# Optimization experiments

Hardware: AMD Instinct MI355X
Metric: run time of the kernel (lower is better)

## Reference

```python
import jax, jax.numpy as jnp
import numpy as np

D_MODEL = 4096
N_HEADS = 32
N_KV_HEADS = 32
D_HEAD = 128
D_LATENT = 512
N_CKV = 4            # n_compressed_kv_heads = d_latent // d_head
T = 2048             # num_tokens (single-sequence prefill)
ROPE_BASE = 10000.0
NEG = -1e30


def _rope(x, positions):
    """Neox-style rotary embedding. x: (T, H, D)."""
    d = x.shape[-1]
    inv_freq = 1.0 / (ROPE_BASE ** (jnp.arange(0, d // 2, dtype=jnp.float32) * (2.0 / d)))
    freqs = positions.astype(jnp.float32)[:, None] * inv_freq[None, :]  # (T, D/2)
    cos = jnp.cos(freqs)[:, None, :]
    sin = jnp.sin(freqs)[:, None, :]
    x1, x2 = jnp.split(x, 2, axis=-1)
    return jnp.concatenate([x1 * cos - x2 * sin, x2 * cos + x1 * sin], axis=-1)


def setup_inputs() -> dict:
    key = jax.random.key(0)
    ks = jax.random.split(key, 6)
    s = jnp.float32(0.02)
    return {
        "positions": jnp.arange(T, dtype=jnp.int32),
        "hidden_states": jax.random.normal(ks[0], (T, D_MODEL), jnp.float32),
        "Wq": jax.random.normal(ks[1], (D_MODEL, N_HEADS * D_HEAD), jnp.float32) * s,
        "Wc": jax.random.normal(ks[2], (D_MODEL, 2 * D_LATENT), jnp.float32) * s,
        "Wuk": jax.random.normal(ks[3], (2 * D_LATENT, N_KV_HEADS * D_HEAD), jnp.float32) * s,
        "Wuv": jax.random.normal(ks[4], (2 * D_LATENT, N_KV_HEADS * D_HEAD), jnp.float32) * s,
        "Wo": jax.random.normal(ks[5], (N_HEADS * D_HEAD, D_MODEL), jnp.float32) * s,
    }


def reference(positions, hidden_states, Wq, Wc, Wuk, Wuv, Wo):
    # Q projection
    q = (hidden_states @ Wq).reshape(T, N_HEADS, D_HEAD)
    # MLA compression: hidden -> c_kv (2*d_latent), split into c_k / c_v
    c_kv = hidden_states @ Wc                                   # (T, 2*D_LATENT)
    c_k = c_kv[:, :D_LATENT].reshape(T, N_CKV, D_HEAD)          # compressed K cache
    c_v = c_kv[:, D_LATENT:].reshape(T, N_CKV, D_HEAD)          # compressed V cache
    # Decompression (computed by the source module; K is RoPE'd then discarded,
    # V is unused -- the v1 attention path runs over the compressed cache).
    K = (c_kv @ Wuk).reshape(T, N_KV_HEADS, D_HEAD)
    V = (c_kv @ Wuv).reshape(T, N_KV_HEADS, D_HEAD)             # noqa: unused, matches source
    # RoPE on q (and K, whose rotated value is dead in the source)
    q = _rope(q, positions)
    K = _rope(K, positions)  # dead, kept for FLOP parity with the source
    # GQA attention: n_heads=32 query heads over n_compressed_kv_heads=4 kv heads
    g = N_HEADS // N_CKV
    qg = q.reshape(T, N_CKV, g, D_HEAD)
    scale = jnp.float32(1.0 / np.sqrt(D_HEAD))
    scores = jnp.einsum('tkgd,skd->kgts', qg, c_k) * scale      # (N_CKV, g, T, T)
    causal = positions[:, None] >= positions[None, :]           # (T, T)
    scores = jnp.where(causal[None, None], scores, NEG)
    probs = jax.nn.softmax(scores, axis=-1)
    ctx = jnp.einsum('kgts,skd->tkgd', probs, c_v).reshape(T, N_HEADS * D_HEAD)
    return ctx @ Wo
```

## Files before the change

### kernel.cpp

```cpp
#include <hip/hip_runtime.h>
#include <hip/hip_bf16.h>
#include <cstdint>
#include <cstddef>


typedef unsigned short u16;
typedef short s16x8 __attribute__((ext_vector_type(8)));
typedef short s16x4 __attribute__((ext_vector_type(4)));
typedef float f32x4 __attribute__((ext_vector_type(4)));

#define MFMA16(a, b, c) __builtin_amdgcn_mfma_f32_16x16x32_bf16((a), (b), (c), 0, 0, 0)

#define QSCALE 0.12751899f
#define LOG2_ROPE_BASE 13.287712379549449f
#define FIXMAX 24.0f

__device__ __forceinline__ u16 f2b(float f) {
  return __builtin_bit_cast(u16, __float2bfloat16(f));
}
__device__ __forceinline__ void async_copy16(u16* lds, const u16* g) {
  __builtin_amdgcn_global_load_lds(
      (const __attribute__((address_space(1))) unsigned int*)g,
      (__attribute__((address_space(3))) unsigned int*)lds, 16, 0, 0);
}

__global__ __launch_bounds__(256)
void prep_kernel(const float* __restrict__ hidden, const float* __restrict__ Wq,
                 const float* __restrict__ Wc, const float* __restrict__ Wo,
                 u16* __restrict__ hb, u16* __restrict__ WqT,
                 u16* __restrict__ WcT, u16* __restrict__ WoT) {
  __shared__ alignas(16) u16 tile[64 * 72];
  const int b = blockIdx.x;
  const int t = threadIdx.x;

  if (b >= 9216) {
    int i = (b - 9216) * 256 + t;
    const float4* p = (const float4*)hidden + (size_t)i * 2;
    float4 a = p[0], c = p[1];
    s16x8 v;
    v[0] = (short)f2b(a.x); v[1] = (short)f2b(a.y);
    v[2] = (short)f2b(a.z); v[3] = (short)f2b(a.w);
    v[4] = (short)f2b(c.x); v[5] = (short)f2b(c.y);
    v[6] = (short)f2b(c.z); v[7] = (short)f2b(c.w);
    *(s16x8*)&hb[(size_t)i * 8] = v;
    return;
  }

  const float* in;
  u16* out;
  int gx, in_ld, out_ld;
  if (b < 4096)      { in = Wq; out = WqT; gx = b;        in_ld = 4096; out_ld = 4096; }
  else if (b < 5120) { in = Wc; out = WcT; gx = b - 4096; in_ld = 1024; out_ld = 4096; }
  else               { in = Wo; out = WoT; gx = b - 5120; in_ld = 4096; out_ld = 4096; }
  const int nbx = in_ld / 64;
  const int c0 = (gx % nbx) * 64, r0 = (gx / nbx) * 64;
  const int rr = t >> 3, cc = (t & 7) * 8;
#pragma unroll
  for (int p = 0; p < 2; p++) {
    int row = p * 32 + rr;
    const float4* src = (const float4*)&in[(size_t)(r0 + row) * in_ld + c0 + cc];
    float4 a = src[0], c = src[1];
    s16x8 v;
    v[0] = (short)f2b(a.x); v[1] = (short)f2b(a.y);
    v[2] = (short)f2b(a.z); v[3] = (short)f2b(a.w);
    v[4] = (short)f2b(c.x); v[5] = (short)f2b(c.y);
    v[6] = (short)f2b(c.z); v[7] = (short)f2b(c.w);
    *(s16x8*)&tile[row * 72 + cc] = v;
  }
  __syncthreads();
#pragma unroll
  for (int p = 0; p < 2; p++) {
    int orow = p * 32 + rr;
    s16x8 v;
#pragma unroll
    for (int j = 0; j < 8; j++) v[j] = (short)tile[(cc + j) * 72 + orow];
    *(s16x8*)&out[(size_t)(c0 + orow) * out_ld + r0 + cc] = v;
  }
}

__global__ __launch_bounds__(256)
void transpose_ckv(const u16* __restrict__ in, u16* __restrict__ out) {
  __shared__ alignas(16) u16 tile[64 * 72];
  const int kh = blockIdx.z;
  const int c0 = blockIdx.x * 64, r0 = blockIdx.y * 64;
  const int in_off = 512 + kh * 128;
  u16* outk = out + (size_t)kh * 128 * 2048;
  const int t = threadIdx.x;
  const int rr = t >> 3, cc = (t & 7) * 8;
#pragma unroll
  for (int p = 0; p < 2; p++) {
    int row = p * 32 + rr;
    s16x8 v = *(const s16x8*)&in[(size_t)(r0 + row) * 1024 + in_off + c0 + cc];
    *(s16x8*)&tile[row * 72 + cc] = v;
  }
  __syncthreads();
#pragma unroll
  for (int p = 0; p < 2; p++) {
    int orow = p * 32 + rr;
    s16x8 v;
#pragma unroll
    for (int j = 0; j < 8; j++) v[j] = (short)tile[(cc + j) * 72 + orow];
    *(s16x8*)&outk[(size_t)(c0 + orow) * 2048 + r0 + cc] = v;
  }
}

template <int EPI>
__global__ __launch_bounds__(256, 3)
void gemm_bt(const u16* __restrict__ A, const u16* __restrict__ Bt,
             void* __restrict__ Cv, void* __restrict__ Cv2,
             const int* __restrict__ positions) {
  __shared__ alignas(16) u16 As[2][128 * 32];
  __shared__ alignas(16) u16 Bs[2][128 * 32];

  const int tid = threadIdx.x;
  const int w = tid >> 6, l = tid & 63;
  const int wm = w >> 1, wn = w & 1;
  const int lrow = l >> 4, lcol = l & 15;

  const int wgid = (int)blockIdx.y * (int)gridDim.x + (int)blockIdx.x;
  const int cpx = (int)gridDim.x >> 3;
  const int xk = wgid & 7, xr = wgid >> 3;
  const int bx = cpx * xk + xr % cpx, by = xr / cpx;
  const int m0 = by * 128, n0 = bx * 128;

  f32x4 acc[4][4] = {};

  const int srow = l >> 2;
  const int scol = ((l & 3) ^ ((l >> 3) & 3)) * 8;
  const int rxor = (lcol >> 1) & 3;
  const u16* Ag = A + (size_t)(m0 + w * 32 + srow) * 4096 + scol;
  const u16* Bg = Bt + (size_t)(n0 + w * 32 + srow) * 4096 + scol;

  for (int kt = 0; kt < 4096; kt += 64) {
    __syncthreads();
#pragma unroll
    for (int hf = 0; hf < 2; hf++) {
      async_copy16(&As[hf][(w * 32) * 32], Ag + kt + hf * 32);
      async_copy16(&As[hf][(w * 32 + 16) * 32],
                   Ag + (size_t)16 * 4096 + kt + hf * 32);
      async_copy16(&Bs[hf][(w * 32) * 32], Bg + kt + hf * 32);
      async_copy16(&Bs[hf][(w * 32 + 16) * 32],
                   Bg + (size_t)16 * 4096 + kt + hf * 32);
    }
    __syncthreads();

#pragma unroll
    for (int hf = 0; hf < 2; hf++) {
      s16x8 a[4], b[4];
#pragma unroll
      for (int i = 0; i < 4; i++)
        a[i] = *(const s16x8*)&As[hf][(wm * 64 + i * 16 + lcol) * 32 +
                                      (lrow ^ rxor) * 8];
#pragma unroll
      for (int j = 0; j < 4; j++)
        b[j] = *(const s16x8*)&Bs[hf][(wn * 32 + (j & 1) * 16 + (j >> 1) * 64 +
                                       lcol) * 32 + (lrow ^ rxor) * 8];
#pragma unroll
      for (int i = 0; i < 4; i++)
#pragma unroll
        for (int j = 0; j < 4; j++)
          acc[i][j] = MFMA16(a[i], b[j], acc[i][j]);
    }
  }

  if constexpr (EPI == 3) {
    float* C = (float*)Cv;
#pragma unroll
    for (int i = 0; i < 4; i++) {
      int row = m0 + wm * 64 + i * 16 + lrow * 4;
#pragma unroll
      for (int j = 0; j < 4; j++) {
        int col = n0 + wn * 32 + (j & 1) * 16 + (j >> 1) * 64 + lcol;
#pragma unroll
        for (int r = 0; r < 4; r++)
          C[(size_t)(row + r) * 4096 + col] = acc[i][j][r];
      }
    }
  } else {
    if (n0 >= 4096) {
      u16* C = (u16*)Cv2;
      int cb = n0 - 4096;
#pragma unroll
      for (int i = 0; i < 4; i++) {
        int row = m0 + wm * 64 + i * 16 + lrow * 4;
#pragma unroll
        for (int j = 0; j < 4; j++) {
          int col = cb + wn * 32 + (j & 1) * 16 + (j >> 1) * 64 + lcol;
#pragma unroll
          for (int r = 0; r < 4; r++)
            C[(size_t)(row + r) * 1024 + col] = f2b(acc[i][j][r]);
        }
      }
    } else {
      u16* C = (u16*)Cv;
      float inv[2];
#pragma unroll
      for (int j = 0; j < 2; j++) {
        int d = wn * 32 + j * 16 + lcol;
        inv[j] = exp2f((float)d * (-LOG2_ROPE_BASE / 64.f));
      }
#pragma unroll
      for (int i = 0; i < 4; i++) {
        int row = m0 + wm * 64 + i * 16 + lrow * 4;
#pragma unroll
        for (int r = 0; r < 4; r++) {
          float pos = (float)positions[row + r];
#pragma unroll
          for (int j = 0; j < 2; j++) {
            int d = wn * 32 + j * 16 + lcol;
            float ang = pos * inv[j];
            float sv, cv;
            sincosf(ang, &sv, &cv);
            float x1 = acc[i][j][r];
            float x2 = acc[i][j + 2][r];
            C[(size_t)(row + r) * 4096 + n0 + d] = f2b((x1 * cv - x2 * sv) * QSCALE);
            C[(size_t)(row + r) * 4096 + n0 + d + 64] =
                f2b((x2 * cv + x1 * sv) * QSCALE);
          }
        }
      }
    }
  }
}

__global__ __launch_bounds__(256, 4)
void attn_kernel(const u16* __restrict__ Q, const u16* __restrict__ ckv,
                 const u16* __restrict__ vT, u16* __restrict__ ctx) {
  __shared__ alignas(16) u16 Kt[2][4096];
  __shared__ alignas(16) u16 Vt[2][4096];
  __shared__ alignas(16) u16 Ps[4][512];

  const int tid = threadIdx.x, w = tid >> 6, l = tid & 63;
  const int lrow = l >> 4, lcol = l & 15;
  const int b = blockIdx.x;
  const int hg = b & 7;
  const int qi = b >> 3;
  const int ji = qi >> 5, ii = qi & 31;
  const int qt = (ji == 0) ? ii : (ji == 1) ? 63 - ii
               : (ji == 2) ? 64 + ii : 127 - ii;
  const int kh = hg >> 1;
  const int h = hg * 4 + w;
  const int nkt = (qt >> 1) + 1;
  const int sxor = (l >> 3) & 3;
  const int kxor = (lcol >> 1) & 3;

  const u16* kg0 = ckv + (size_t)(l >> 2) * 1024 + kh * 128 + w * 32 +
                   ((l & 3) ^ sxor) * 8;
  const u16* vg0 = vT + (size_t)(kh * 128 + w * 32 + (l >> 2)) * 2048 +
                   ((l & 3) ^ sxor) * 8;

  s16x8 qf[4];
  {
    const u16* qg = Q + (size_t)(qt * 16 + lcol) * 4096 + h * 128 + lrow * 8;
#pragma unroll
    for (int kc = 0; kc < 4; kc++)
      qf[kc] = *(const s16x8*)&qg[kc * 32];
  }

  f32x4 o[8] = {};
  float lsum = 0.f;

  {
    async_copy16(&Kt[0][w * 1024], kg0);
    async_copy16(&Kt[0][w * 1024 + 512], kg0 + (size_t)16 * 1024);
    async_copy16(&Vt[0][w * 1024], vg0);
    async_copy16(&Vt[0][w * 1024 + 512], vg0 + (size_t)16 * 2048);
  }
  asm volatile("s_waitcnt vmcnt(0)" ::: "memory");
  __syncthreads();

#pragma unroll 1
  for (int kt = 0; kt < nkt; kt++) {
    const int cur = kt & 1;
    if (kt + 1 < nkt) {
      const u16* kg = kg0 + (size_t)(kt + 1) * 32 * 1024;
      const u16* vg = vg0 + (size_t)(kt + 1) * 32;
      async_copy16(&Kt[cur ^ 1][w * 1024], kg);
      async_copy16(&Kt[cur ^ 1][w * 1024 + 512], kg + (size_t)16 * 1024);
      async_copy16(&Vt[cur ^ 1][w * 1024], vg);
      async_copy16(&Vt[cur ^ 1][w * 1024 + 512], vg + (size_t)16 * 2048);
    }

    f32x4 s[2] = {};
    __builtin_amdgcn_s_setprio(1);
#pragma unroll
    for (int kc = 0; kc < 4; kc++) {
#pragma unroll
      for (int mt = 0; mt < 2; mt++) {
        s16x8 ka = *(const s16x8*)&Kt[cur][kc * 1024 + (mt * 16 + lcol) * 32 +
                                          (lrow ^ kxor) * 8];
        s[mt] = MFMA16(ka, qf[kc], s[mt]);
      }
    }
    __builtin_amdgcn_s_setprio(0);

    if (kt == nkt - 1) {
      const int qloc = (qt & 1) * 16 + lcol;
#pragma unroll
      for (int mt = 0; mt < 2; mt++)
#pragma unroll
        for (int r = 0; r < 4; r++) {
          int key = mt * 16 + lrow * 4 + r;
          if (key > qloc) s[mt][r] = -1e30f;
        }
    }

#pragma unroll
    for (int mt = 0; mt < 2; mt++) {
      s16x4 pk;
#pragma unroll
      for (int r = 0; r < 4; r++) {
        float p = exp2f(s[mt][r] - FIXMAX);
        lsum += p;
        pk[r] = (short)f2b(p);
      }
      const int key32 = mt * 16 + lrow * 4;
      *(s16x4*)&Ps[w][lcol * 32 + (key32 ^ (kxor << 3))] = pk;
    }

    s16x8 pa = *(const s16x8*)&Ps[w][lcol * 32 + (lrow ^ kxor) * 8];
    __builtin_amdgcn_s_setprio(1);
#pragma unroll
    for (int ntO = 0; ntO < 8; ntO++) {
      s16x8 vb = *(const s16x8*)&Vt[cur][(ntO * 16 + lcol) * 32 +
                                         (lrow ^ kxor) * 8];
      o[ntO] = MFMA16(pa, vb, o[ntO]);
    }
    __builtin_amdgcn_s_setprio(0);

    asm volatile("s_waitcnt vmcnt(0)" ::: "memory");
    __syncthreads();
  }

  lsum += __shfl_xor(lsum, 16);
  lsum += __shfl_xor(lsum, 32);
  float* fl = (float*)&Ps[w][0];
  if (l < 16) fl[l] = 1.f / lsum;
  f32x4 lf = *(const f32x4*)&fl[lrow * 4];
#pragma unroll
  for (int ntO = 0; ntO < 8; ntO++)
#pragma unroll
    for (int r = 0; r < 4; r++) {
      int q = qt * 16 + lrow * 4 + r;
      int d = h * 128 + ntO * 16 + lcol;
      ctx[(size_t)q * 4096 + d] = f2b(o[ntO][r] * lf[r]);
    }
}

extern "C" void kernel_launch(void* const* d_in, const int* in_sizes, int n_in,
                              void* d_out, int out_size, void* d_ws, size_t ws_size,
                              hipStream_t stream) {
  const int* positions = (const int*)d_in[0];
  const float* hidden = (const float*)d_in[1];
  const float* Wq = (const float*)d_in[2];
  const float* Wc = (const float*)d_in[3];
  const float* Wo = (const float*)d_in[6];

  char* ws = (char*)d_ws;
  u16* hb  = (u16*)(ws);
  u16* WT  = (u16*)(ws + 16777216);
  u16* qbf = (u16*)(ws + 58720256);
  u16* ckv = (u16*)(ws + 75497472);
  u16* cvT = (u16*)(ws + 79691776);
  u16* WoT = (u16*)(ws + 81788928);
  u16* ctx = hb;

  dim3 blk(256);

  prep_kernel<<<dim3(13312), blk, 0, stream>>>(hidden, Wq, Wc, Wo, hb, WT,
                                               WT + (size_t)4096 * 4096, WoT);

  gemm_bt<1><<<dim3(40, 16), blk, 0, stream>>>(hb, WT, qbf, ckv, positions);

  transpose_ckv<<<dim3(2, 32, 4), blk, 0, stream>>>(ckv, cvT);

  attn_kernel<<<dim3(1024), blk, 0, stream>>>(qbf, ckv, cvT, ctx);

  gemm_bt<3><<<dim3(32, 16), blk, 0, stream>>>(ctx, WoT, d_out, nullptr,
                                               positions);
}
```

Baseline: 458.3 us.

## Replace GEMM with 256x256 8-wave pipelined kernel and fuse cV transpose

Rewrites the projection GEMMs as a 512-thread kernel with 256x256 tiles, double-buffered async LDS staging in four k/m sub-phases with explicit vmcnt waits, and MFMA priority raising. The first GEMM's epilogue now writes the V half of c_kv transposed straight into cvT, so the separate transpose kernel launch goes away. The aim is more data reuse per tile and overlap of loads with MFMA work. In exchange, grids become small (160 and 128 blocks) against the device's compute-unit count, which may leave units idle and cause tail effects.

After: 518.8 us. 1.13x slower.

```diff
diff --git a/kernel.cpp b/kernel.cpp
--- a/kernel.cpp
+++ b/kernel.cpp
@@ -78,114 +78,159 @@
   }
 }
 
-__global__ __launch_bounds__(256)
-void transpose_ckv(const u16* __restrict__ in, u16* __restrict__ out) {
-  __shared__ alignas(16) u16 tile[64 * 72];
-  const int kh = blockIdx.z;
-  const int c0 = blockIdx.x * 64, r0 = blockIdx.y * 64;
-  const int in_off = 512 + kh * 128;
-  u16* outk = out + (size_t)kh * 128 * 2048;
-  const int t = threadIdx.x;
-  const int rr = t >> 3, cc = (t & 7) * 8;
-#pragma unroll
-  for (int p = 0; p < 2; p++) {
-    int row = p * 32 + rr;
-    s16x8 v = *(const s16x8*)&in[(size_t)(r0 + row) * 1024 + in_off + c0 + cc];
-    *(s16x8*)&tile[row * 72 + cc] = v;
-  }
-  __syncthreads();
-#pragma unroll
-  for (int p = 0; p < 2; p++) {
-    int orow = p * 32 + rr;
-    s16x8 v;
-#pragma unroll
-    for (int j = 0; j < 8; j++) v[j] = (short)tile[(cc + j) * 72 + orow];
-    *(s16x8*)&outk[(size_t)(c0 + orow) * 2048 + r0 + cc] = v;
-  }
-}
-
 template <int EPI>
-__global__ __launch_bounds__(256, 3)
-void gemm_bt(const u16* __restrict__ A, const u16* __restrict__ Bt,
-             void* __restrict__ Cv, void* __restrict__ Cv2,
-             const int* __restrict__ positions) {
-  __shared__ alignas(16) u16 As[2][128 * 32];
-  __shared__ alignas(16) u16 Bs[2][128 * 32];
+__global__ __launch_bounds__(512, 2)
+void gemm8(const u16* __restrict__ A, const u16* __restrict__ Bt,
+           void* __restrict__ Cv, void* __restrict__ Cv2,
+           u16* __restrict__ CvT, const int* __restrict__ positions) {
+  __shared__ alignas(16) u16 As[2][2][256 * 32];
+  __shared__ alignas(16) u16 Bs[2][2][256 * 32];
 
   const int tid = threadIdx.x;
   const int w = tid >> 6, l = tid & 63;
-  const int wm = w >> 1, wn = w & 1;
+  const int wm = w >> 2, wn = w & 3;
   const int lrow = l >> 4, lcol = l & 15;
-
-  const int wgid = (int)blockIdx.y * (int)gridDim.x + (int)blockIdx.x;
-  const int cpx = (int)gridDim.x >> 3;
-  const int xk = wgid & 7, xr = wgid >> 3;
-  const int bx = cpx * xk + xr % cpx, by = xr / cpx;
-  const int m0 = by * 128, n0 = bx * 128;
-
-  f32x4 acc[4][4] = {};
-
-  const int srow = l >> 2;
-  const int scol = ((l & 3) ^ ((l >> 3) & 3)) * 8;
+  const int wgid = (int)blockIdx.x;
+  const int by = wgid & 7, bx = wgid >> 3;
+  const int m0 = by * 256, n0 = bx * 256;
   const int rxor = (lcol >> 1) & 3;
-  const u16* Ag = A + (size_t)(m0 + w * 32 + srow) * 4096 + scol;
-  const u16* Bg = Bt + (size_t)(n0 + w * 32 + srow) * 4096 + scol;
-
-  for (int kt = 0; kt < 4096; kt += 64) {
-    __syncthreads();
-#pragma unroll
-    for (int hf = 0; hf < 2; hf++) {
-      async_copy16(&As[hf][(w * 32) * 32], Ag + kt + hf * 32);
-      async_copy16(&As[hf][(w * 32 + 16) * 32],
-                   Ag + (size_t)16 * 4096 + kt + hf * 32);
-      async_copy16(&Bs[hf][(w * 32) * 32], Bg + kt + hf * 32);
-      async_copy16(&Bs[hf][(w * 32 + 16) * 32],
-                   Bg + (size_t)16 * 4096 + kt + hf * 32);
-    }
-    __syncthreads();
-
-#pragma unroll
-    for (int hf = 0; hf < 2; hf++) {
-      s16x8 a[4], b[4];
-#pragma unroll
-      for (int i = 0; i < 4; i++)
-        a[i] = *(const s16x8*)&As[hf][(wm * 64 + i * 16 + lcol) * 32 +
-                                      (lrow ^ rxor) * 8];
-#pragma unroll
-      for (int j = 0; j < 4; j++)
-        b[j] = *(const s16x8*)&Bs[hf][(wn * 32 + (j & 1) * 16 + (j >> 1) * 64 +
-                                       lcol) * 32 + (lrow ^ rxor) * 8];
-#pragma unroll
-      for (int i = 0; i < 4; i++)
-#pragma unroll
-        for (int j = 0; j < 4; j++)
-          acc[i][j] = MFMA16(a[i], b[j], acc[i][j]);
-    }
+
+  f32x4 acc[8][4] = {};
+
+  const int srow = tid >> 2;
+  const int schunk = ((tid & 3) ^ ((tid >> 3) & 3)) * 8;
+  const u16* Ag = A + (size_t)(m0 + srow) * 4096 + schunk;
+  const u16* Bg = Bt + (size_t)(n0 + srow) * 4096 + schunk;
+
+#define STAGE_AQ(buf, kp, mh, kt)                                         \
+  async_copy16(&As[buf][kp][(mh)*4096 + tid * 8],                         \
+               Ag + (size_t)(mh)*128 * 4096 + (kt) + (kp)*32)
+#define STAGE_B(buf, kp, kt)                                              \
+  do {                                                                    \
+    async_copy16(&Bs[buf][kp][tid * 8], Bg + (kt) + (kp)*32);             \
+    async_copy16(&Bs[buf][kp][4096 + tid * 8],                            \
+                 Bg + (size_t)128 * 4096 + (kt) + (kp)*32);               \
+  } while (0)
+#define WAITBAR(N)                                                        \
+  asm volatile("s_waitcnt vmcnt(" #N ")\n\ts_barrier" ::: "memory");      \
+  __builtin_amdgcn_sched_barrier(0)
+
+  STAGE_AQ(0, 0, 0, 0);
+  STAGE_B(0, 0, 0);
+  STAGE_AQ(0, 0, 1, 0);
+  STAGE_AQ(0, 1, 0, 0);
+  STAGE_B(0, 1, 0);
+  STAGE_AQ(0, 1, 1, 0);
+
+#pragma unroll 1
+  for (int t = 0; t < 64; t++) {
+    const int buf = t & 1;
+    const int nb = buf ^ 1;
+    const int kt2 = (t + 1) * 64;
+    const bool last = (t == 63);
+
+#define PHASE_BODY(kp, mh)                                                \
+  s16x8 a0, a1, a2, a3, b0, b1, b2, b3;                                   \
+  {                                                                       \
+    const u16* Ap = &As[buf][kp][0];                                      \
+    const u16* Bp = &Bs[buf][kp][0];                                      \
+    const int ar = (wm * 128 + (mh)*64 + lcol) * 32 + (lrow ^ rxor) * 8;  \
+    const int br = (wn * 16 + lcol) * 32 + (lrow ^ rxor) * 8;             \
+    a0 = *(const s16x8*)&Ap[ar];                                          \
+    a1 = *(const s16x8*)&Ap[ar + 16 * 32];                                \
+    a2 = *(const s16x8*)&Ap[ar + 32 * 32];                                \
+    a3 = *(const s16x8*)&Ap[ar + 48 * 32];                                \
+    b0 = *(const s16x8*)&Bp[br];                                          \
+    b1 = *(const s16x8*)&Bp[br + 64 * 32];                                \
+    b2 = *(const s16x8*)&Bp[br + 128 * 32];                               \
+    b3 = *(const s16x8*)&Bp[br + 192 * 32];                               \
+  }
+#define PHASE_MFMA(kp, mh)                                                \
+  asm volatile("s_waitcnt lgkmcnt(0)" ::: "memory");                      \
+  __builtin_amdgcn_sched_barrier(0);                                      \
+  __builtin_amdgcn_s_setprio(1);                                          \
+  acc[(mh)*4 + 0][0] = MFMA16(a0, b0, acc[(mh)*4 + 0][0]);                \
+  acc[(mh)*4 + 0][1] = MFMA16(a0, b1, acc[(mh)*4 + 0][1]);                \
+  acc[(mh)*4 + 0][2] = MFMA16(a0, b2, acc[(mh)*4 + 0][2]);                \
+  acc[(mh)*4 + 0][3] = MFMA16(a0, b3, acc[(mh)*4 + 0][3]);                \
+  acc[(mh)*4 + 1][0] = MFMA16(a1, b0, acc[(mh)*4 + 1][0]);                \
+  acc[(mh)*4 + 1][1] = MFMA16(a1, b1, acc[(mh)*4 + 1][1]);                \
+  acc[(mh)*4 + 1][2] = MFMA16(a1, b2, acc[(mh)*4 + 1][2]);                \
+  acc[(mh)*4 + 1][3] = MFMA16(a1, b3, acc[(mh)*4 + 1][3]);                \
+  acc[(mh)*4 + 2][0] = MFMA16(a2, b0, acc[(mh)*4 + 2][0]);                \
+  acc[(mh)*4 + 2][1] = MFMA16(a2, b1, acc[(mh)*4 + 2][1]);                \
+  acc[(mh)*4 + 2][2] = MFMA16(a2, b2, acc[(mh)*4 + 2][2]);                \
+  acc[(mh)*4 + 2][3] = MFMA16(a2, b3, acc[(mh)*4 + 2][3]);                \
+  acc[(mh)*4 + 3][0] = MFMA16(a3, b0, acc[(mh)*4 + 3][0]);                \
+  acc[(mh)*4 + 3][1] = MFMA16(a3, b1, acc[(mh)*4 + 3][1]);                \
+  acc[(mh)*4 + 3][2] = MFMA16(a3, b2, acc[(mh)*4 + 3][2]);                \
+  acc[(mh)*4 + 3][3] = MFMA16(a3, b3, acc[(mh)*4 + 3][3]);                \
+  __builtin_amdgcn_s_setprio(0)
+
+    {
+      WAITBAR(5);
+      PHASE_BODY(0, 0)
+      if (!last) { STAGE_AQ(nb, 0, 0, kt2); STAGE_B(nb, 0, kt2); }
+      PHASE_MFMA(0, 0);
+    }
+    {
+      if (!last) { WAITBAR(7); } else { WAITBAR(4); }
+      PHASE_BODY(0, 1)
+      if (!last) { STAGE_AQ(nb, 0, 1, kt2); }
+      PHASE_MFMA(0, 1);
+    }
+    {
+      if (!last) { WAITBAR(5); } else { WAITBAR(1); }
+      PHASE_BODY(1, 0)
+      if (!last) { STAGE_AQ(nb, 1, 0, kt2); STAGE_B(nb, 1, kt2); }
+      PHASE_MFMA(1, 0);
+    }
+    {
+      if (!last) { WAITBAR(7); } else { WAITBAR(0); }
+      PHASE_BODY(1, 1)
+      if (!last) { STAGE_AQ(nb, 1, 1, kt2); }
+      PHASE_MFMA(1, 1);
+    }
+#undef PHASE_BODY
+#undef PHASE_MFMA
   }
 
   if constexpr (EPI == 3) {
     float* C = (float*)Cv;
 #pragma unroll
-    for (int i = 0; i < 4; i++) {
-      int row = m0 + wm * 64 + i * 16 + lrow * 4;
+    for (int i = 0; i < 8; i++) {
+      int row = m0 + wm * 128 + i * 16 + lrow * 4;
 #pragma unroll
       for (int j = 0; j < 4; j++) {
-        int col = n0 + wn * 32 + (j & 1) * 16 + (j >> 1) * 64 + lcol;
+        int col = n0 + j * 64 + wn * 16 + lcol;
 #pragma unroll
         for (int r = 0; r < 4; r++)
           C[(size_t)(row + r) * 4096 + col] = acc[i][j][r];
       }
     }
   } else {
-    if (n0 >= 4096) {
+    if (n0 >= 4608) {
+#pragma unroll
+      for (int i = 0; i < 8; i++) {
+        int row = m0 + wm * 128 + i * 16 + lrow * 4;
+#pragma unroll
+        for (int j = 0; j < 4; j++) {
+          int c = n0 - 4608 + j * 64 + wn * 16 + lcol;
+          s16x4 pk;
+#pragma unroll
+          for (int r = 0; r < 4; r++) pk[r] = (short)f2b(acc[i][j][r]);
+          *(s16x4*)&CvT[(size_t)c * 2048 + row] = pk;
+        }
+      }
+    } else if (n0 >= 4096) {
       u16* C = (u16*)Cv2;
       int cb = n0 - 4096;
 #pragma unroll
-      for (int i = 0; i < 4; i++) {
-        int row = m0 + wm * 64 + i * 16 + lrow * 4;
+      for (int i = 0; i < 8; i++) {
+        int row = m0 + wm * 128 + i * 16 + lrow * 4;
 #pragma unroll
         for (int j = 0; j < 4; j++) {
-          int col = cb + wn * 32 + (j & 1) * 16 + (j >> 1) * 64 + lcol;
+          int col = cb + j * 64 + wn * 16 + lcol;
 #pragma unroll
           for (int r = 0; r < 4; r++)
             C[(size_t)(row + r) * 1024 + col] = f2b(acc[i][j][r]);
@@ -193,34 +238,31 @@
       }
     } else {
       u16* C = (u16*)Cv;
-      float inv[2];
-#pragma unroll
-      for (int j = 0; j < 2; j++) {
-        int d = wn * 32 + j * 16 + lcol;
-        inv[j] = exp2f((float)d * (-LOG2_ROPE_BASE / 64.f));
-      }
-#pragma unroll
-      for (int i = 0; i < 4; i++) {
-        int row = m0 + wm * 64 + i * 16 + lrow * 4;
+      const int d = wn * 16 + lcol;
+      const float inv = exp2f((float)d * (-LOG2_ROPE_BASE / 64.f));
+#pragma unroll
+      for (int i = 0; i < 8; i++) {
+        int row = m0 + wm * 128 + i * 16 + lrow * 4;
 #pragma unroll
         for (int r = 0; r < 4; r++) {
           float pos = (float)positions[row + r];
-#pragma unroll
-          for (int j = 0; j < 2; j++) {
-            int d = wn * 32 + j * 16 + lcol;
-            float ang = pos * inv[j];
-            float sv, cv;
-            sincosf(ang, &sv, &cv);
-            float x1 = acc[i][j][r];
-            float x2 = acc[i][j + 2][r];
-            C[(size_t)(row + r) * 4096 + n0 + d] = f2b((x1 * cv - x2 * sv) * QSCALE);
-            C[(size_t)(row + r) * 4096 + n0 + d + 64] =
-                f2b((x2 * cv + x1 * sv) * QSCALE);
+          float sv, cv;
+          sincosf(pos * inv, &sv, &cv);
+#pragma unroll
+          for (int jp = 0; jp < 2; jp++) {
+            float x1 = acc[i][jp * 2][r];
+            float x2 = acc[i][jp * 2 + 1][r];
+            size_t base = (size_t)(row + r) * 4096 + n0 + jp * 128 + d;
+            C[base] = f2b((x1 * cv - x2 * sv) * QSCALE);
+            C[base + 64] = f2b((x2 * cv + x1 * sv) * QSCALE);
           }
         }
       }
     }
   }
+#undef STAGE_AQ
+#undef STAGE_B
+#undef WAITBAR
 }
 
 __global__ __launch_bounds__(256, 4)
@@ -365,17 +407,13 @@
   u16* WoT = (u16*)(ws + 81788928);
   u16* ctx = hb;
 
-  dim3 blk(256);
-
-  prep_kernel<<<dim3(13312), blk, 0, stream>>>(hidden, Wq, Wc, Wo, hb, WT,
-                                               WT + (size_t)4096 * 4096, WoT);
-
-  gemm_bt<1><<<dim3(40, 16), blk, 0, stream>>>(hb, WT, qbf, ckv, positions);
-
-  transpose_ckv<<<dim3(2, 32, 4), blk, 0, stream>>>(ckv, cvT);
-
-  attn_kernel<<<dim3(1024), blk, 0, stream>>>(qbf, ckv, cvT, ctx);
-
-  gemm_bt<3><<<dim3(32, 16), blk, 0, stream>>>(ctx, WoT, d_out, nullptr,
-                                               positions);
-}
+  prep_kernel<<<dim3(13312), dim3(256), 0, stream>>>(hidden, Wq, Wc, Wo, hb, WT,
+                                                     WT + (size_t)4096 * 4096, WoT);
+
+  gemm8<1><<<dim3(160), dim3(512), 0, stream>>>(hb, WT, qbf, ckv, cvT, positions);
+
+  attn_kernel<<<dim3(1024), dim3(256), 0, stream>>>(qbf, ckv, cvT, ctx);
+
+  gemm8<3><<<dim3(128), dim3(512), 0, stream>>>(ctx, WoT, d_out, nullptr,
+                                                nullptr, positions);
+}
```

## Triple-buffer GEMM K-loop with async prefetch and fuse c_v transpose into epilogue

Applied to the files above, without the earlier changes.

Replaces the GEMM main loop's load-then-compute double-half structure with a three-stage LDS ring: two stages are prefetched up front, and each iteration waits only for the oldest stage (vmcnt(4)) before issuing the next prefetch, so global-to-LDS copies overlap the MFMAs. The c_v half of the compression output is now written transposed straight from the GEMM epilogue as packed bf16x4 stores, which removes the separate transpose kernel launch and its extra read/write pass. The cost is more LDS per block (3 stages instead of 2), which may lower occupancy under the launch-bounds hint. The transposed stores are strided by 2048 elements, so they are poorly coalesced.

Measured after the change: 480.6 us. 4.9% more time.

```diff
diff --git a/kernel.cpp b/kernel.cpp
--- a/kernel.cpp
+++ b/kernel.cpp
@@ -78,39 +78,13 @@
   }
 }
 
-__global__ __launch_bounds__(256)
-void transpose_ckv(const u16* __restrict__ in, u16* __restrict__ out) {
-  __shared__ alignas(16) u16 tile[64 * 72];
-  const int kh = blockIdx.z;
-  const int c0 = blockIdx.x * 64, r0 = blockIdx.y * 64;
-  const int in_off = 512 + kh * 128;
-  u16* outk = out + (size_t)kh * 128 * 2048;
-  const int t = threadIdx.x;
-  const int rr = t >> 3, cc = (t & 7) * 8;
-#pragma unroll
-  for (int p = 0; p < 2; p++) {
-    int row = p * 32 + rr;
-    s16x8 v = *(const s16x8*)&in[(size_t)(r0 + row) * 1024 + in_off + c0 + cc];
-    *(s16x8*)&tile[row * 72 + cc] = v;
-  }
-  __syncthreads();
-#pragma unroll
-  for (int p = 0; p < 2; p++) {
-    int orow = p * 32 + rr;
-    s16x8 v;
-#pragma unroll
-    for (int j = 0; j < 8; j++) v[j] = (short)tile[(cc + j) * 72 + orow];
-    *(s16x8*)&outk[(size_t)(c0 + orow) * 2048 + r0 + cc] = v;
-  }
-}
-
 template <int EPI>
 __global__ __launch_bounds__(256, 3)
 void gemm_bt(const u16* __restrict__ A, const u16* __restrict__ Bt,
              void* __restrict__ Cv, void* __restrict__ Cv2,
-             const int* __restrict__ positions) {
-  __shared__ alignas(16) u16 As[2][128 * 32];
-  __shared__ alignas(16) u16 Bs[2][128 * 32];
+             u16* __restrict__ CvT, const int* __restrict__ positions) {
+  __shared__ alignas(16) u16 As[3][128 * 32];
+  __shared__ alignas(16) u16 Bs[3][128 * 32];
 
   const int tid = threadIdx.x;
   const int w = tid >> 6, l = tid & 63;
@@ -131,37 +105,47 @@
   const u16* Ag = A + (size_t)(m0 + w * 32 + srow) * 4096 + scol;
   const u16* Bg = Bt + (size_t)(n0 + w * 32 + srow) * 4096 + scol;
 
-  for (int kt = 0; kt < 4096; kt += 64) {
-    __syncthreads();
-#pragma unroll
-    for (int hf = 0; hf < 2; hf++) {
-      async_copy16(&As[hf][(w * 32) * 32], Ag + kt + hf * 32);
-      async_copy16(&As[hf][(w * 32 + 16) * 32],
-                   Ag + (size_t)16 * 4096 + kt + hf * 32);
-      async_copy16(&Bs[hf][(w * 32) * 32], Bg + kt + hf * 32);
-      async_copy16(&Bs[hf][(w * 32 + 16) * 32],
-                   Bg + (size_t)16 * 4096 + kt + hf * 32);
-    }
-    __syncthreads();
-
-#pragma unroll
-    for (int hf = 0; hf < 2; hf++) {
-      s16x8 a[4], b[4];
-#pragma unroll
-      for (int i = 0; i < 4; i++)
-        a[i] = *(const s16x8*)&As[hf][(wm * 64 + i * 16 + lcol) * 32 +
-                                      (lrow ^ rxor) * 8];
+#define STAGE(buf, kt)                                                     \
+  do {                                                                     \
+    async_copy16(&As[buf][(w * 32) * 32], Ag + (kt));                      \
+    async_copy16(&As[buf][(w * 32 + 16) * 32],                             \
+                 Ag + (size_t)16 * 4096 + (kt));                           \
+    async_copy16(&Bs[buf][(w * 32) * 32], Bg + (kt));                      \
+    async_copy16(&Bs[buf][(w * 32 + 16) * 32],                             \
+                 Bg + (size_t)16 * 4096 + (kt));                           \
+  } while (0)
+
+  STAGE(0, 0);
+  STAGE(1, 32);
+
+#pragma unroll 1
+  for (int t = 0; t < 128; t++) {
+    const int cb_ = t % 3;
+    if (t == 127) {
+      asm volatile("s_waitcnt vmcnt(0)\n\ts_barrier" ::: "memory");
+    } else {
+      asm volatile("s_waitcnt vmcnt(4)\n\ts_barrier" ::: "memory");
+    }
+    if (t + 2 < 128) STAGE((t + 2) % 3, (t + 2) * 32);
+
+    s16x8 a[4], b[4];
+#pragma unroll
+    for (int i = 0; i < 4; i++)
+      a[i] = *(const s16x8*)&As[cb_][(wm * 64 + i * 16 + lcol) * 32 +
+                                     (lrow ^ rxor) * 8];
+#pragma unroll
+    for (int j = 0; j < 4; j++)
+      b[j] = *(const s16x8*)&Bs[cb_][(wn * 32 + (j & 1) * 16 + (j >> 1) * 64 +
+                                      lcol) * 32 + (lrow ^ rxor) * 8];
+#pragma unroll
+    for (int i = 0; i < 4; i++)
 #pragma unroll
       for (int j = 0; j < 4; j++)
-        b[j] = *(const s16x8*)&Bs[hf][(wn * 32 + (j & 1) * 16 + (j >> 1) * 64 +
-                                       lcol) * 32 + (lrow ^ rxor) * 8];
-#pragma unroll
-      for (int i = 0; i < 4; i++)
-#pragma unroll
-        for (int j = 0; j < 4; j++)
-          acc[i][j] = MFMA16(a[i], b[j], acc[i][j]);
-    }
-  }
+        acc[i][j] = MFMA16(a[i], b[j], acc[i][j]);
+
+    asm volatile("s_waitcnt lgkmcnt(0)" ::: "memory");
+  }
+#undef STAGE
 
   if constexpr (EPI == 3) {
     float* C = (float*)Cv;
@@ -177,7 +161,20 @@
       }
     }
   } else {
-    if (n0 >= 4096) {
+    if (n0 >= 4608) {
+#pragma unroll
+      for (int i = 0; i < 4; i++) {
+        int row = m0 + wm * 64 + i * 16 + lrow * 4;
+#pragma unroll
+        for (int j = 0; j < 4; j++) {
+          int c = n0 - 4608 + wn * 32 + (j & 1) * 16 + (j >> 1) * 64 + lcol;
+          s16x4 pk;
+#pragma unroll
+          for (int r = 0; r < 4; r++) pk[r] = (short)f2b(acc[i][j][r]);
+          *(s16x4*)&CvT[(size_t)c * 2048 + row] = pk;
+        }
+      }
+    } else if (n0 >= 4096) {
       u16* C = (u16*)Cv2;
       int cb = n0 - 4096;
 #pragma unroll
@@ -370,12 +367,10 @@
   prep_kernel<<<dim3(13312), blk, 0, stream>>>(hidden, Wq, Wc, Wo, hb, WT,
                                                WT + (size_t)4096 * 4096, WoT);
 
-  gemm_bt<1><<<dim3(40, 16), blk, 0, stream>>>(hb, WT, qbf, ckv, positions);
-
-  transpose_ckv<<<dim3(2, 32, 4), blk, 0, stream>>>(ckv, cvT);
+  gemm_bt<1><<<dim3(40, 16), blk, 0, stream>>>(hb, WT, qbf, ckv, cvT, positions);
 
   attn_kernel<<<dim3(1024), blk, 0, stream>>>(qbf, ckv, cvT, ctx);
 
   gemm_bt<3><<<dim3(32, 16), blk, 0, stream>>>(ctx, WoT, d_out, nullptr,
-                                               positions);
-}
+                                               nullptr, positions);
+}
```
